# Performance work log

Hardware: AMD Instinct MI355X
Metric: run time of the kernel (lower is better)

## Reference

```python
import jax, jax.numpy as jnp
import numpy as np

B, T, D, H = 1, 4096, 1024, 16
HD = D // H          # head_dim = 64
W_LOCAL = 256        # sliding-window half-width (hardcoded in module)
N_GLOBAL = 64        # number of global tokens (hardcoded in module)


def setup_inputs() -> dict:
    key = jax.random.key(0)
    ks = jax.random.split(key, 7)
    s = 0.02
    return {
        "hidden_states": jax.random.normal(ks[0], (B, T, D), dtype=jnp.float32),
        "Wqkv": jax.random.normal(ks[1], (D, 3 * D), dtype=jnp.float32) * s,
        "bqkv": jnp.zeros((3 * D,), dtype=jnp.float32),
        "Wout": jax.random.normal(ks[2], (D, D), dtype=jnp.float32) * s,
        "bout": jnp.zeros((D,), dtype=jnp.float32),
        "Wg": jax.random.normal(ks[3], (D, 1), dtype=jnp.float32) * s,
        "bg": jnp.zeros((1,), dtype=jnp.float32),
    }


def reference(hidden_states, Wqkv, bqkv, Wout, bout, Wg, bg):
    b, t, d = hidden_states.shape
    scale = 1.0 / jnp.sqrt(jnp.asarray(HD, hidden_states.dtype))

    qkv = hidden_states @ Wqkv + bqkv                     # [B,T,3D]
    q, k, v = jnp.split(qkv, 3, axis=-1)
    # [B,T,D] -> [B,H,T,HD]
    q, k, v = (x.reshape(b, t, H, HD).transpose(0, 2, 1, 3) for x in (q, k, v))

    # local sliding-window attention (dense scores masked to |i-j| <= w, as in source)
    idx = jnp.arange(t)
    local_mask = jnp.abs(idx[None, :] - idx[:, None]) <= W_LOCAL   # [T,T]
    scores = jnp.einsum('bhqd,bhkd->bhqk', q, k) * scale           # [B,H,T,T]
    scores = jnp.where(local_mask[None, None], scores, -jnp.inf)
    attn_local = jnp.einsum('bhqk,bhkd->bhqd', jax.nn.softmax(scores, axis=-1), v)

    # global-token attention: every query attends to the first N_GLOBAL tokens
    ng = min(N_GLOBAL, t)
    k_g = k[:, :, :ng, :]                                          # [B,H,G,HD]
    v_g = v[:, :, :ng, :]
    scores_g = jnp.einsum('bhqd,bhgd->bhqg', q, k_g) * scale       # [B,H,T,G]
    attn_global = jnp.einsum('bhqg,bhgd->bhqd', jax.nn.softmax(scores_g, axis=-1), v_g)

    # sigmoid gate combine, broadcast over heads and head_dim
    gate = jax.nn.sigmoid(hidden_states @ Wg + bg).reshape(b, 1, t, 1)
    out = (1.0 - gate) * attn_local + gate * attn_global           # [B,H,T,HD]
    out = out.transpose(0, 2, 1, 3).reshape(b, t, d)
    return out @ Wout + bout
```

## Files before the change

kernel.cpp:

```cpp
#include <hip/hip_runtime.h>

typedef _Float16 half8 __attribute__((ext_vector_type(8)));
typedef _Float16 half4_t __attribute__((ext_vector_type(4)));
typedef float f32x4 __attribute__((ext_vector_type(4)));

#define MFMA(a, b, c) __builtin_amdgcn_mfma_f32_16x16x32_f16(a, b, c, 0, 0, 0)

constexpr int T_TOK = 4096;
constexpr int DMODEL = 1024;
constexpr int WLOC = 256;

typedef const __attribute__((address_space(1))) uint32_t* gptr_t;
typedef __attribute__((address_space(3))) uint32_t* lptr_t;
static __device__ __forceinline__ void gl16(const void* g, void* l) {
  __builtin_amdgcn_global_load_lds((gptr_t)g, (lptr_t)l, 16, 0, 0);
}

__global__ __launch_bounds__(256) void k_cast(const float* __restrict__ in,
                                              _Float16* __restrict__ out) {
  int i = (blockIdx.x * 256 + threadIdx.x) * 8;
  f32x4 a = *(const f32x4*)(in + i);
  f32x4 b = *(const f32x4*)(in + i + 4);
  half8 h;
  h[0] = (_Float16)a[0]; h[1] = (_Float16)a[1]; h[2] = (_Float16)a[2]; h[3] = (_Float16)a[3];
  h[4] = (_Float16)b[0]; h[5] = (_Float16)b[1]; h[6] = (_Float16)b[2]; h[7] = (_Float16)b[3];
  *(half8*)(out + i) = h;
}

__global__ __launch_bounds__(256) void k_transpose_cast(const float* __restrict__ in,
                                                        _Float16* __restrict__ out,
                                                        int R, int C) {
  __shared__ float tile[64][65];
  int r0 = blockIdx.y * 64, c0 = blockIdx.x * 64;
  int tr = threadIdx.x >> 4;
  int tc = (threadIdx.x & 15) * 4;
#pragma unroll
  for (int p = 0; p < 4; ++p) {
    int r = p * 16 + tr;
    f32x4 v = *(const f32x4*)&in[(size_t)(r0 + r) * C + c0 + tc];
    tile[r][tc + 0] = v[0]; tile[r][tc + 1] = v[1];
    tile[r][tc + 2] = v[2]; tile[r][tc + 3] = v[3];
  }
  __syncthreads();
#pragma unroll
  for (int p = 0; p < 4; ++p) {
    int c = p * 16 + tr;
    half4_t h;
    h[0] = (_Float16)tile[tc + 0][c];
    h[1] = (_Float16)tile[tc + 1][c];
    h[2] = (_Float16)tile[tc + 2][c];
    h[3] = (_Float16)tile[tc + 3][c];
    *(half4_t*)&out[(size_t)(c0 + c) * R + r0 + tc] = h;
  }
}

__global__ __launch_bounds__(256) void k_gate(const float* __restrict__ hs,
                                              const float* __restrict__ Wg,
                                              const float* __restrict__ bg,
                                              float* __restrict__ gate) {
  int t = blockIdx.x * 4 + (threadIdx.x >> 6);
  int lane = threadIdx.x & 63;
  float s = 0.f;
#pragma unroll
  for (int i = 0; i < 16; ++i)
    s += hs[(size_t)t * DMODEL + lane + i * 64] * Wg[lane + i * 64];
#pragma unroll
  for (int off = 32; off; off >>= 1) s += __shfl_xor(s, off);
  if (lane == 0) gate[t] = 1.f / (1.f + __expf(-(s + bg[0])));
}

template <int MODE>
__global__ __launch_bounds__(256) void k_gemm(const _Float16* __restrict__ A,
                                              const _Float16* __restrict__ Bt,
                                              const float* __restrict__ bias,
                                              float* __restrict__ Cout,
                                              _Float16* __restrict__ qh,
                                              _Float16* __restrict__ kh,
                                              _Float16* __restrict__ vt,
                                              int M, int N, int K) {
  __shared__ __align__(16) _Float16 As[128][32];
  __shared__ __align__(16) _Float16 Bs[128][32];
  int tid = threadIdx.x;
  int lane = tid & 63, wave = tid >> 6;
  int wm = wave >> 1, wn = wave & 1;
  int m0 = blockIdx.y * 128, n0 = blockIdx.x * 128;
  int lr = lane & 15, lk = (lane >> 4) * 8;
  int sr = tid >> 2, sc = (tid & 3) * 8;
  f32x4 acc[4][4] = {};

  for (int kt = 0; kt < K; kt += 32) {
    __syncthreads();
    gl16(&A[(size_t)(m0 + sr) * K + kt + sc],       &As[sr][sc]);
    gl16(&A[(size_t)(m0 + sr + 64) * K + kt + sc],  &As[sr + 64][sc]);
    gl16(&Bt[(size_t)(n0 + sr) * K + kt + sc],      &Bs[sr][sc]);
    gl16(&Bt[(size_t)(n0 + sr + 64) * K + kt + sc], &Bs[sr + 64][sc]);
    __syncthreads();
    half8 af[4], bf[4];
#pragma unroll
    for (int i = 0; i < 4; ++i) af[i] = *(half8*)&As[wm * 64 + i * 16 + lr][lk];
#pragma unroll
    for (int i = 0; i < 4; ++i) bf[i] = *(half8*)&Bs[wn * 64 + i * 16 + lr][lk];
#pragma unroll
    for (int i = 0; i < 4; ++i)
#pragma unroll
      for (int j = 0; j < 4; ++j)
        acc[i][j] = MFMA(af[i], bf[j], acc[i][j]);
  }

  int lg2 = lane >> 4;
#pragma unroll
  for (int j = 0; j < 4; ++j) {
    int n = n0 + wn * 64 + j * 16 + lr;
    float b = bias[n];
#pragma unroll
    for (int i = 0; i < 4; ++i) {
#pragma unroll
      for (int r = 0; r < 4; ++r) {
        int m = m0 + wm * 64 + i * 16 + lg2 * 4 + r;
        float v = acc[i][j][r] + b;
        if (MODE == 1) {
          Cout[(size_t)m * N + n] = v;
        } else {
          int hh = (n >> 6) & 15, d = n & 63;
          if (n < 1024)      qh[((size_t)hh * T_TOK + m) * 64 + d] = (_Float16)v;
          else if (n < 2048) kh[((size_t)hh * T_TOK + m) * 64 + d] = (_Float16)v;
          else               vt[((size_t)hh * 64 + d) * T_TOK + m] = (_Float16)v;
        }
      }
    }
  }
}

__global__ __launch_bounds__(256) void k_attn(const _Float16* __restrict__ q_all,
                                              const _Float16* __restrict__ k_all,
                                              const _Float16* __restrict__ vT_all,
                                              const float* __restrict__ gate,
                                              _Float16* __restrict__ attn_h) {
  __shared__ __align__(16) _Float16 Ks[64][72];
  __shared__ __align__(16) _Float16 Vs[64][72];
  __shared__ __align__(16) _Float16 P[4][16][72];

  int n = blockIdx.x;
  int o = (n & 7) * 128 + (n >> 3);
  int h = o >> 6, qb = o & 63;
  int q0 = qb * 64;
  int tid = threadIdx.x;
  int lane = tid & 63, w = tid >> 6;
  int lr = lane & 15, lgp = lane >> 4;

  const _Float16* qh = q_all + (size_t)h * T_TOK * 64;
  const _Float16* kh = k_all + (size_t)h * T_TOK * 64;
  const _Float16* vt = vT_all + (size_t)h * 64 * T_TOK;

  half8 aq0 = *(const half8*)&qh[(size_t)(q0 + w * 16 + lr) * 64 + lgp * 8];
  half8 aq1 = *(const half8*)&qh[(size_t)(q0 + w * 16 + lr) * 64 + 32 + lgp * 8];
#pragma unroll
  for (int j = 0; j < 8; ++j) { aq0[j] = aq0[j] * (_Float16)0.125f; aq1[j] = aq1[j] * (_Float16)0.125f; }

  int r8 = tid >> 3, c8 = (tid & 7) * 8;
  half8 kr0, kr1, vr0, vr1;

  auto ldregs = [&](int key0) {
    kr0 = *(const half8*)&kh[(size_t)(key0 + r8) * 64 + c8];
    kr1 = *(const half8*)&kh[(size_t)(key0 + r8 + 32) * 64 + c8];
    vr0 = *(const half8*)&vt[(size_t)r8 * T_TOK + key0 + c8];
    vr1 = *(const half8*)&vt[(size_t)(r8 + 32) * T_TOK + key0 + c8];
  };
  auto dswrite = [&]() {
    *(half8*)&Ks[r8][c8]      = kr0;
    *(half8*)&Ks[r8 + 32][c8] = kr1;
    *(half8*)&Vs[r8][c8]      = vr0;
    *(half8*)&Vs[r8 + 32][c8] = vr1;
  };

  f32x4 acc_g[4] = {}, acc_l[4] = {};
  float m_g = -1e30f, l_g = 0.f, m_l = -1e30f, l_l = 0.f;

  auto compute = [&](int key0, bool use_mask, f32x4 (&acc)[4], float& ms, float& ls) {
    f32x4 s[4] = {};
#pragma unroll
    for (int g = 0; g < 4; ++g) {
      half8 b0 = *(half8*)&Ks[g * 16 + lr][lgp * 8];
      half8 b1 = *(half8*)&Ks[g * 16 + lr][32 + lgp * 8];
      s[g] = MFMA(b0, aq0, s[g]);
      s[g] = MFMA(b1, aq1, s[g]);
    }
    if (use_mask) {
      int moff = key0 + lgp * 4 - (q0 + w * 16 + lr) + WLOC;
#pragma unroll
      for (int g = 0; g < 4; ++g)
#pragma unroll
        for (int r = 0; r < 4; ++r) {
          unsigned u = (unsigned)(moff + g * 16 + r);
          if (u > 2u * WLOC) s[g][r] = -1e30f;
        }
    }
    float mloc = -1e30f;
#pragma unroll
    for (int g = 0; g < 4; ++g)
#pragma unroll
      for (int r = 0; r < 4; ++r) mloc = fmaxf(mloc, s[g][r]);
    mloc = fmaxf(mloc, __shfl_xor(mloc, 16));
    mloc = fmaxf(mloc, __shfl_xor(mloc, 32));
    if (__any(mloc > ms)) {
      float mn = fmaxf(ms, mloc);
      float al = __expf(ms - mn);
      ms = mn;
      float alr[4];
#pragma unroll
      for (int r = 0; r < 4; ++r) alr[r] = __shfl(al, lgp * 4 + r);
#pragma unroll
      for (int dt = 0; dt < 4; ++dt)
#pragma unroll
        for (int r = 0; r < 4; ++r) acc[dt][r] *= alr[r];
      ls *= al;
    }
    float rsum = 0.f;
#pragma unroll
    for (int g = 0; g < 4; ++g)
#pragma unroll
      for (int r = 0; r < 4; ++r) {
        float p = __expf(s[g][r] - ms);
        s[g][r] = p;
        rsum += p;
      }
    rsum += __shfl_xor(rsum, 16);
    rsum += __shfl_xor(rsum, 32);
    ls += rsum;
#pragma unroll
    for (int g = 0; g < 4; ++g) {
      half4_t q4;
      q4[0] = (_Float16)s[g][0]; q4[1] = (_Float16)s[g][1];
      q4[2] = (_Float16)s[g][2]; q4[3] = (_Float16)s[g][3];
      *(half4_t*)&P[w][lr][g * 16 + lgp * 4] = q4;
    }
    half8 pa0 = *(half8*)&P[w][lr][lgp * 8];
    half8 pa1 = *(half8*)&P[w][lr][32 + lgp * 8];
#pragma unroll
    for (int dt = 0; dt < 4; ++dt) {
      half8 bv0 = *(half8*)&Vs[dt * 16 + lr][lgp * 8];
      half8 bv1 = *(half8*)&Vs[dt * 16 + lr][32 + lgp * 8];
      acc[dt] = MFMA(pa0, bv0, acc[dt]);
      acc[dt] = MFMA(pa1, bv1, acc[dt]);
    }
  };

  ldregs(0);
  dswrite();
  __syncthreads();
  int lo = q0 - WLOC; if (lo < 0) lo = 0;
  int hi = q0 + 63 + WLOC + 1; if (hi > T_TOK) hi = T_TOK;
  ldregs(lo);
  compute(0, false, acc_g, m_g, l_g);
  __syncthreads();
  dswrite();
  __syncthreads();

  for (int key0 = lo; key0 < hi; key0 += 64) {
    int nxt = key0 + 64;
    bool have_nxt = nxt < hi;
    if (have_nxt) ldregs(nxt);
    bool use_mask = (key0 < q0 - 192) || (key0 > q0 + 192);
    compute(key0, use_mask, acc_l, m_l, l_l);
    __syncthreads();
    if (have_nxt) { dswrite(); __syncthreads(); }
  }

  float llr[4], lgr[4];
#pragma unroll
  for (int r = 0; r < 4; ++r) {
    llr[r] = __shfl(l_l, lgp * 4 + r);
    lgr[r] = __shfl(l_g, lgp * 4 + r);
  }
#pragma unroll
  for (int r = 0; r < 4; ++r) {
    int q = q0 + w * 16 + lgp * 4 + r;
    float g = gate[q];
#pragma unroll
    for (int dt = 0; dt < 4; ++dt) {
      float o2 = (1.f - g) * (acc_l[dt][r] / llr[r]) + g * (acc_g[dt][r] / lgr[r]);
      attn_h[(size_t)q * DMODEL + h * 64 + dt * 16 + lr] = (_Float16)o2;
    }
  }
}

extern "C" void kernel_launch(void* const* d_in, const int* in_sizes, int n_in,
                              void* d_out, int out_size, void* d_ws, size_t ws_size,
                              hipStream_t stream) {
  const float* hs   = (const float*)d_in[0];
  const float* Wqkv = (const float*)d_in[1];
  const float* bqkv = (const float*)d_in[2];
  const float* Wout = (const float*)d_in[3];
  const float* bout = (const float*)d_in[4];
  const float* Wg   = (const float*)d_in[5];
  const float* bg   = (const float*)d_in[6];
  float* out = (float*)d_out;

  char* ws = (char*)d_ws;
  _Float16* hidden_h = (_Float16*)(ws);
  _Float16* Wqkv_t   = (_Float16*)(ws + 8388608);
  _Float16* Wout_t   = (_Float16*)(ws + 14680064);
  _Float16* q_h      = (_Float16*)(ws + 16777216);
  _Float16* k_h      = (_Float16*)(ws + 25165824);
  _Float16* vT_h     = (_Float16*)(ws + 33554432);
  float*    gate     = (float*)(ws + 41943040);
  _Float16* attn_h   = hidden_h;

  k_cast<<<2048, 256, 0, stream>>>(hs, hidden_h);
  k_gate<<<1024, 256, 0, stream>>>(hs, Wg, bg, gate);
  k_transpose_cast<<<dim3(48, 16), 256, 0, stream>>>(Wqkv, Wqkv_t, 1024, 3072);
  k_transpose_cast<<<dim3(16, 16), 256, 0, stream>>>(Wout, Wout_t, 1024, 1024);
  k_gemm<0><<<dim3(24, 32), 256, 0, stream>>>(hidden_h, Wqkv_t, bqkv, nullptr,
                                              q_h, k_h, vT_h, 4096, 3072, 1024);
  k_attn<<<1024, 256, 0, stream>>>(q_h, k_h, vT_h, gate, attn_h);
  k_gemm<1><<<dim3(8, 32), 256, 0, stream>>>(attn_h, Wout_t, bout, out,
                                             nullptr, nullptr, nullptr, 4096, 1024, 1024);
}
```

Baseline: 200.1 us.

## Double-buffer GEMM LDS tiles, remap workgroups across XCDs, fuse cast with gate

The GEMM kernel now uses two LDS buffers and prefetches the next K tile while computing the current one, cutting one barrier per iteration. Workgroup IDs are remapped so consecutive tiles land on the same XCD for better L2 reuse, using a 1D grid. The fp16 cast of hidden states and the gate dot product are merged into one kernel that reads the input once. It doubles LDS use per block, which may reduce occupancy.

Measured after the change: 185.5 us. 1.08x faster.

```diff
diff --git a/kernel.cpp b/kernel.cpp
--- a/kernel.cpp
+++ b/kernel.cpp
@@ -16,15 +16,30 @@
   __builtin_amdgcn_global_load_lds((gptr_t)g, (lptr_t)l, 16, 0, 0);
 }
 
-__global__ __launch_bounds__(256) void k_cast(const float* __restrict__ in,
-                                              _Float16* __restrict__ out) {
-  int i = (blockIdx.x * 256 + threadIdx.x) * 8;
-  f32x4 a = *(const f32x4*)(in + i);
-  f32x4 b = *(const f32x4*)(in + i + 4);
-  half8 h;
-  h[0] = (_Float16)a[0]; h[1] = (_Float16)a[1]; h[2] = (_Float16)a[2]; h[3] = (_Float16)a[3];
-  h[4] = (_Float16)b[0]; h[5] = (_Float16)b[1]; h[6] = (_Float16)b[2]; h[7] = (_Float16)b[3];
-  *(half8*)(out + i) = h;
+__global__ __launch_bounds__(256) void k_castgate(const float* __restrict__ hs,
+                                                  const float* __restrict__ Wg,
+                                                  const float* __restrict__ bg,
+                                                  _Float16* __restrict__ out,
+                                                  float* __restrict__ gate) {
+  int w = threadIdx.x >> 6, lane = threadIdx.x & 63;
+  int t = blockIdx.x * 4 + w;
+  const float* row = hs + (size_t)t * DMODEL;
+  _Float16* orow = out + (size_t)t * DMODEL;
+  float s = 0.f;
+#pragma unroll
+  for (int i = 0; i < 4; ++i) {
+    int off = lane * 4 + i * 256;
+    f32x4 v = *(const f32x4*)(row + off);
+    f32x4 g = *(const f32x4*)(Wg + off);
+    s += v[0] * g[0] + v[1] * g[1] + v[2] * g[2] + v[3] * g[3];
+    half4_t h;
+    h[0] = (_Float16)v[0]; h[1] = (_Float16)v[1];
+    h[2] = (_Float16)v[2]; h[3] = (_Float16)v[3];
+    *(half4_t*)(orow + off) = h;
+  }
+#pragma unroll
+  for (int off = 32; off; off >>= 1) s += __shfl_xor(s, off);
+  if (lane == 0) gate[t] = 1.f / (1.f + __expf(-(s + bg[0])));
 }
 
 __global__ __launch_bounds__(256) void k_transpose_cast(const float* __restrict__ in,
@@ -54,22 +69,7 @@
   }
 }
 
-__global__ __launch_bounds__(256) void k_gate(const float* __restrict__ hs,
-                                              const float* __restrict__ Wg,
-                                              const float* __restrict__ bg,
-                                              float* __restrict__ gate) {
-  int t = blockIdx.x * 4 + (threadIdx.x >> 6);
-  int lane = threadIdx.x & 63;
-  float s = 0.f;
-#pragma unroll
-  for (int i = 0; i < 16; ++i)
-    s += hs[(size_t)t * DMODEL + lane + i * 64] * Wg[lane + i * 64];
-#pragma unroll
-  for (int off = 32; off; off >>= 1) s += __shfl_xor(s, off);
-  if (lane == 0) gate[t] = 1.f / (1.f + __expf(-(s + bg[0])));
-}
-
-template <int MODE>
+template <int MODE, int NBX>
 __global__ __launch_bounds__(256) void k_gemm(const _Float16* __restrict__ A,
                                               const _Float16* __restrict__ Bt,
                                               const float* __restrict__ bias,
@@ -78,33 +78,46 @@
                                               _Float16* __restrict__ kh,
                                               _Float16* __restrict__ vt,
                                               int M, int N, int K) {
-  __shared__ __align__(16) _Float16 As[128][32];
-  __shared__ __align__(16) _Float16 Bs[128][32];
+  __shared__ __align__(16) _Float16 As[2][128][32];
+  __shared__ __align__(16) _Float16 Bs[2][128][32];
+  int nwg = gridDim.x;
+  int cpx = nwg >> 3;
+  int orig = blockIdx.x;
+  int wg = (orig & 7) * cpx + (orig >> 3);
+  int bx = wg % NBX, by = wg / NBX;
+  int m0 = by * 128, n0 = bx * 128;
+
   int tid = threadIdx.x;
   int lane = tid & 63, wave = tid >> 6;
   int wm = wave >> 1, wn = wave & 1;
-  int m0 = blockIdx.y * 128, n0 = blockIdx.x * 128;
   int lr = lane & 15, lk = (lane >> 4) * 8;
   int sr = tid >> 2, sc = (tid & 3) * 8;
   f32x4 acc[4][4] = {};
 
+  auto stage = [&](int kt, int b) {
+    gl16(&A[(size_t)(m0 + sr) * K + kt + sc],       &As[b][sr][sc]);
+    gl16(&A[(size_t)(m0 + sr + 64) * K + kt + sc],  &As[b][sr + 64][sc]);
+    gl16(&Bt[(size_t)(n0 + sr) * K + kt + sc],      &Bs[b][sr][sc]);
+    gl16(&Bt[(size_t)(n0 + sr + 64) * K + kt + sc], &Bs[b][sr + 64][sc]);
+  };
+
+  stage(0, 0);
+  __syncthreads();
+  int cur = 0;
   for (int kt = 0; kt < K; kt += 32) {
-    __syncthreads();
-    gl16(&A[(size_t)(m0 + sr) * K + kt + sc],       &As[sr][sc]);
-    gl16(&A[(size_t)(m0 + sr + 64) * K + kt + sc],  &As[sr + 64][sc]);
-    gl16(&Bt[(size_t)(n0 + sr) * K + kt + sc],      &Bs[sr][sc]);
-    gl16(&Bt[(size_t)(n0 + sr + 64) * K + kt + sc], &Bs[sr + 64][sc]);
-    __syncthreads();
+    if (kt + 32 < K) stage(kt + 32, cur ^ 1);
     half8 af[4], bf[4];
 #pragma unroll
-    for (int i = 0; i < 4; ++i) af[i] = *(half8*)&As[wm * 64 + i * 16 + lr][lk];
-#pragma unroll
-    for (int i = 0; i < 4; ++i) bf[i] = *(half8*)&Bs[wn * 64 + i * 16 + lr][lk];
+    for (int i = 0; i < 4; ++i) af[i] = *(half8*)&As[cur][wm * 64 + i * 16 + lr][lk];
+#pragma unroll
+    for (int i = 0; i < 4; ++i) bf[i] = *(half8*)&Bs[cur][wn * 64 + i * 16 + lr][lk];
 #pragma unroll
     for (int i = 0; i < 4; ++i)
 #pragma unroll
       for (int j = 0; j < 4; ++j)
         acc[i][j] = MFMA(af[i], bf[j], acc[i][j]);
+    __syncthreads();
+    cur ^= 1;
   }
 
   int lg2 = lane >> 4;
@@ -306,13 +319,12 @@
   float*    gate     = (float*)(ws + 41943040);
   _Float16* attn_h   = hidden_h;
 
-  k_cast<<<2048, 256, 0, stream>>>(hs, hidden_h);
-  k_gate<<<1024, 256, 0, stream>>>(hs, Wg, bg, gate);
+  k_castgate<<<1024, 256, 0, stream>>>(hs, Wg, bg, hidden_h, gate);
   k_transpose_cast<<<dim3(48, 16), 256, 0, stream>>>(Wqkv, Wqkv_t, 1024, 3072);
   k_transpose_cast<<<dim3(16, 16), 256, 0, stream>>>(Wout, Wout_t, 1024, 1024);
-  k_gemm<0><<<dim3(24, 32), 256, 0, stream>>>(hidden_h, Wqkv_t, bqkv, nullptr,
-                                              q_h, k_h, vT_h, 4096, 3072, 1024);
+  k_gemm<0, 24><<<768, 256, 0, stream>>>(hidden_h, Wqkv_t, bqkv, nullptr,
+                                         q_h, k_h, vT_h, 4096, 3072, 1024);
   k_attn<<<1024, 256, 0, stream>>>(q_h, k_h, vT_h, gate, attn_h);
-  k_gemm<1><<<dim3(8, 32), 256, 0, stream>>>(attn_h, Wout_t, bout, out,
-                                             nullptr, nullptr, nullptr, 4096, 1024, 1024);
-}
+  k_gemm<1, 8><<<256, 256, 0, stream>>>(attn_h, Wout_t, bout, out,
+                                        nullptr, nullptr, nullptr, 4096, 1024, 1024);
+}
```
